# Performance work log

Measured on AMD Instinct MI355X. Metric: run time of the kernel, lower is better.

The kernel has to match this reference:

```python
import jax, jax.numpy as jnp
import numpy as np

B, S, D, H, F, L = 4, 2048, 768, 12, 3072, 4
DH = D // H  # dim_head = 64
EPS = 1e-5


def _layernorm(x, g, b):
    mu = jnp.mean(x, axis=-1, keepdims=True)
    var = jnp.var(x, axis=-1, keepdims=True)
    return (x - mu) * jax.lax.rsqrt(var + EPS) * g + b


def setup_inputs() -> dict:
    key = jax.random.key(0)
    ks = jax.random.split(key, 12)
    sc = 0.02
    x = jax.random.normal(ks[0], (B, S, D), dtype=jnp.float32)
    # causal mask: True where attention is disallowed (j > i)
    causal = jnp.triu(jnp.ones((S, S), dtype=bool), k=1)
    attn_mask = jnp.broadcast_to(causal, (B, S, S))
    Wq = jax.random.normal(ks[1], (L, D, D), dtype=jnp.float32) * sc
    Wk = jax.random.normal(ks[2], (L, D, D), dtype=jnp.float32) * sc
    Wv = jax.random.normal(ks[3], (L, D, D), dtype=jnp.float32) * sc
    Wo = jax.random.normal(ks[4], (L, D, D), dtype=jnp.float32) * sc
    bo = jnp.zeros((L, D), dtype=jnp.float32)
    ln1_g = jnp.ones((L, D), dtype=jnp.float32)
    ln1_b = jnp.zeros((L, D), dtype=jnp.float32)
    W1 = jax.random.normal(ks[5], (L, D, F), dtype=jnp.float32) * sc
    b1 = jnp.zeros((L, F), dtype=jnp.float32)
    W2 = jax.random.normal(ks[6], (L, F, D), dtype=jnp.float32) * sc
    b2 = jnp.zeros((L, D), dtype=jnp.float32)
    ln2_g = jnp.ones((L, D), dtype=jnp.float32)
    ln2_b = jnp.zeros((L, D), dtype=jnp.float32)
    return dict(x=x, attn_mask=attn_mask, Wq=Wq, Wk=Wk, Wv=Wv, Wo=Wo, bo=bo,
                ln1_g=ln1_g, ln1_b=ln1_b, W1=W1, b1=b1, W2=W2, b2=b2,
                ln2_g=ln2_g, ln2_b=ln2_b)


def _decoder_layer(x, mask, Wq, Wk, Wv, Wo, bo, ln1_g, ln1_b, W1, b1, W2, b2, ln2_g, ln2_b):
    # multi-head attention (dropout = identity in eval)
    q = (x @ Wq).reshape(B, S, H, DH).transpose(0, 2, 1, 3)  # (B,H,S,DH)
    k = (x @ Wk).reshape(B, S, H, DH).transpose(0, 2, 1, 3)
    v = (x @ Wv).reshape(B, S, H, DH).transpose(0, 2, 1, 3)
    a = jnp.einsum('bhqd,bhkd->bhqk', q, k) / jnp.sqrt(jnp.float32(DH))
    a = jnp.where(mask[:, None, :, :], jnp.float32(-1e9), a)
    p = jax.nn.softmax(a, axis=-1)
    av = jnp.einsum('bhqk,bhkd->bhqd', p, v)
    av = av.transpose(0, 2, 1, 3).reshape(B, S, D)
    attn_out = av @ Wo + bo
    h = _layernorm(x + attn_out, ln1_g, ln1_b)
    # FFN: Conv1d(kernel=1) == pointwise linear; exact GELU (torch F.gelu default)
    f = jax.nn.gelu(h @ W1 + b1, approximate=False) @ W2 + b2
    return _layernorm(h + f, ln2_g, ln2_b)


def reference(x, attn_mask, Wq, Wk, Wv, Wo, bo, ln1_g, ln1_b, W1, b1, W2, b2, ln2_g, ln2_b):
    for l in range(L):
        x = _decoder_layer(x, attn_mask, Wq[l], Wk[l], Wv[l], Wo[l], bo[l],
                           ln1_g[l], ln1_b[l], W1[l], b1[l], W2[l], b2[l],
                           ln2_g[l], ln2_b[l])
    return x
```

## Files before the change

kernel.cpp:

```cpp
#include <hip/hip_runtime.h>
#include <hip/hip_bf16.h>
#include <math.h>

#define BB 4
#define SS 2048
#define DD 768
#define HH 12
#define DHD 64
#define FF 3072
#define LL 4

typedef float f4 __attribute__((ext_vector_type(4)));
typedef float ffrag __attribute__((ext_vector_type(4)));
typedef __bf16 bf16x8 __attribute__((ext_vector_type(8)));
typedef __bf16 bf16x4 __attribute__((ext_vector_type(4)));

__device__ __forceinline__ void gld_lds16(const __bf16* g, __bf16* l) {
  __builtin_amdgcn_global_load_lds(
      (const __attribute__((address_space(1))) void*)g,
      (__attribute__((address_space(3))) void*)l, 16, 0, 0);
}

__device__ __forceinline__ float gelu_f(float x) {
  const float x2 = x * x;
  const float e = __expf(x * fmaf(-0.0713548162f, x2, -1.5957691216f));
  return x / (1.f + e);
}

template <int ACT, int WRITE_BF16, int MODE>
__global__ __launch_bounds__(256) void gemm_mfma(
    const __bf16* __restrict__ A,
    const __bf16* __restrict__ Bt,
    const float* __restrict__ bias,
    float* __restrict__ Cf,
    __bf16* __restrict__ Cb,
    __bf16* __restrict__ Vt,
    int M, int N, int K) {
  __shared__ __bf16 As[128 * 64];
  __shared__ __bf16 Bs[128 * 64];
  const int tid = threadIdx.x;
  const int lane = tid & 63;
  const int wid = tid >> 6;
  const int m0 = blockIdx.y * 128;
  const int n0 = blockIdx.x * 128;
  const int wm = (wid >> 1) * 64;
  const int wn = (wid & 1) * 64;

  ffrag acc[4][4];
#pragma unroll
  for (int i = 0; i < 4; ++i)
#pragma unroll
    for (int j = 0; j < 4; ++j) acc[i][j] = (ffrag)0.f;

  const int kr = lane >> 4;
  const int ml = lane & 15;
  const int quad = lane >> 4;

  for (int k0 = 0; k0 < K; k0 += 64) {
    __syncthreads();
#pragma unroll
    for (int it = 0; it < 4; ++it) {
      const int gidx = it * 256 + wid * 64 + lane;
      const int row = gidx >> 3;
      const int gl = (gidx & 7) ^ (row & 7);
      gld_lds16(A + (size_t)(m0 + row) * K + k0 + gl * 8,
                As + (size_t)(it * 256 + wid * 64) * 8);
      gld_lds16(Bt + (size_t)(n0 + row) * K + k0 + gl * 8,
                Bs + (size_t)(it * 256 + wid * 64) * 8);
    }
    __syncthreads();

#pragma unroll
    for (int kh = 0; kh < 64; kh += 32) {
      const int gb = (kh >> 3) + kr;
      bf16x8 af[4], bfr[4];
#pragma unroll
      for (int i = 0; i < 4; ++i) {
        const int ra = wm + i * 16 + ml;
        af[i] = *(const bf16x8*)(As + ra * 64 + ((gb ^ (ra & 7)) * 8));
        const int rb = wn + i * 16 + ml;
        bfr[i] = *(const bf16x8*)(Bs + rb * 64 + ((gb ^ (rb & 7)) * 8));
      }
#pragma unroll
      for (int i = 0; i < 4; ++i)
#pragma unroll
        for (int j = 0; j < 4; ++j) {
          if (MODE == 2)
            acc[i][j] = __builtin_amdgcn_mfma_f32_16x16x32_bf16(
                af[i], bfr[j], acc[i][j], 0, 0, 0);
          else
            acc[i][j] = __builtin_amdgcn_mfma_f32_16x16x32_bf16(
                bfr[j], af[i], acc[i][j], 0, 0, 0);
        }
    }
  }

  if (MODE == 2) {
    const int rq = quad * 4;
#pragma unroll
    for (int j = 0; j < 4; ++j) {
      const int col = n0 + wn + j * 16 + ml;
      const int hh = col >> 6, d = col & 63;
#pragma unroll
      for (int i = 0; i < 4; ++i) {
        const int row = m0 + wm + i * 16 + rq;
        const int bi = row >> 11, s = row & 2047;
        bf16x4 pk;
#pragma unroll
        for (int r = 0; r < 4; ++r) pk[r] = (__bf16)acc[i][j][r];
        *(bf16x4*)(Vt + ((size_t)(bi * HH + hh) * DHD + d) * SS + s) = pk;
      }
    }
  } else {
#pragma unroll
    for (int j = 0; j < 4; ++j) {
      const int ncol = n0 + wn + j * 16 + quad * 4;
      float4 b4 = make_float4(0.f, 0.f, 0.f, 0.f);
      if (MODE == 0 && bias) b4 = *(const float4*)(bias + ncol);
#pragma unroll
      for (int i = 0; i < 4; ++i) {
        const int mrow = m0 + wm + i * 16 + ml;
        float v0 = acc[i][j][0] + b4.x;
        float v1 = acc[i][j][1] + b4.y;
        float v2 = acc[i][j][2] + b4.z;
        float v3 = acc[i][j][3] + b4.w;
        if (ACT) {
          v0 = gelu_f(v0); v1 = gelu_f(v1);
          v2 = gelu_f(v2); v3 = gelu_f(v3);
        }
        if (MODE == 1) {
          bf16x4 pk;
          pk[0] = (__bf16)v0; pk[1] = (__bf16)v1;
          pk[2] = (__bf16)v2; pk[3] = (__bf16)v3;
          *(bf16x4*)(Cb + (size_t)mrow * 1536 + ncol) = pk;
        } else if (WRITE_BF16) {
          bf16x4 pk;
          pk[0] = (__bf16)v0; pk[1] = (__bf16)v1;
          pk[2] = (__bf16)v2; pk[3] = (__bf16)v3;
          *(bf16x4*)(Cb + (size_t)mrow * N + ncol) = pk;
        } else {
          float4 o; o.x = v0; o.y = v1; o.z = v2; o.w = v3;
          *(float4*)(Cf + (size_t)mrow * N + ncol) = o;
        }
      }
    }
  }
}

__global__ __launch_bounds__(256) void wtrans_kernel(
    const float* __restrict__ src, __bf16* __restrict__ dst, int R, int C,
    size_t src_ls, size_t dst_ls) {
  __shared__ float t[32][33];
  src += (size_t)blockIdx.z * src_ls;
  dst += (size_t)blockIdx.z * dst_ls;
  const int tx = threadIdx.x & 31;
  const int ty = threadIdx.x >> 5;
  const int r0 = blockIdx.y * 32;
  const int c0 = blockIdx.x * 32;
#pragma unroll
  for (int i = 0; i < 4; ++i)
    t[ty + i * 8][tx] = src[(size_t)(r0 + ty + i * 8) * C + c0 + tx];
  __syncthreads();
#pragma unroll
  for (int i = 0; i < 4; ++i)
    dst[(size_t)(c0 + ty + i * 8) * R + r0 + tx] = (__bf16)t[tx][ty + i * 8];
}

__global__ __launch_bounds__(256) void cvt_kernel(
    const float* __restrict__ x, __bf16* __restrict__ y, int n4) {
  const int i = blockIdx.x * 256 + threadIdx.x;
  if (i < n4) {
    const float4 v = *(const float4*)(x + (size_t)i * 4);
    bf16x4 o;
    o[0] = (__bf16)v.x; o[1] = (__bf16)v.y;
    o[2] = (__bf16)v.z; o[3] = (__bf16)v.w;
    *(bf16x4*)(y + (size_t)i * 4) = o;
  }
}

__global__ __launch_bounds__(256, 3) void attn_mfma(
    const __bf16* __restrict__ QK, const __bf16* __restrict__ VT,
    __bf16* __restrict__ O) {
  __shared__ __bf16 qs[64 * 64];
  __shared__ __bf16 ks[2][64 * 64];
  __shared__ __bf16 vts[2][64 * 64];
  __shared__ __bf16 ps[64 * 72];

  const int h = blockIdx.y;
  const int b = blockIdx.z;
  const int tid = threadIdx.x;
  const int lane = tid & 63;
  const int wid = tid >> 6;
  const int ml = lane & 15;
  const int quad = lane >> 4;
  const int wq = wid * 16;
  const size_t rowbase = (size_t)b * SS;
  const int hc = h * 64;
  const size_t vbase = (size_t)(b * HH + h) * DHD;
  const int NT = SS / 64;

  const int gidx0 = wid * 64 + lane;
  const int row0 = gidx0 >> 3;
  const int gl0 = (gidx0 & 7) ^ (row0 & 7);
  const int gidx1 = 256 + wid * 64 + lane;
  const int row1 = gidx1 >> 3;
  const int gl1 = (gidx1 & 7) ^ (row1 & 7);

  for (int ph = 0; ph < 2; ++ph) {
    const int qt = ph ? (NT - 1 - (int)blockIdx.x) : (int)blockIdx.x;
    const int q0 = qt * 64;

    __syncthreads();

    gld_lds16(QK + (rowbase + q0 + row0) * 1536 + hc + gl0 * 8,
              qs + (size_t)(wid * 64) * 8);
    gld_lds16(QK + (rowbase + q0 + row1) * 1536 + hc + gl1 * 8,
              qs + (size_t)(256 + wid * 64) * 8);
    gld_lds16(QK + (rowbase + row0) * 1536 + 768 + hc + gl0 * 8,
              ks[0] + (size_t)(wid * 64) * 8);
    gld_lds16(QK + (rowbase + row1) * 1536 + 768 + hc + gl1 * 8,
              ks[0] + (size_t)(256 + wid * 64) * 8);
    gld_lds16(VT + (vbase + row0) * SS + gl0 * 8, vts[0] + (size_t)(wid * 64) * 8);
    gld_lds16(VT + (vbase + row1) * SS + gl1 * 8, vts[0] + (size_t)(256 + wid * 64) * 8);

    ffrag oacc[4];
#pragma unroll
    for (int d = 0; d < 4; ++d) oacc[d] = (ffrag)0.f;
    float l_acc = 0.f;

    for (int ch = 0; ch <= qt; ++ch) {
      const int j0 = ch * 64;
      const int cur = ch & 1;
      __syncthreads();

      if (ch < qt) {
        const int jn = j0 + 64;
        gld_lds16(QK + (rowbase + jn + row0) * 1536 + 768 + hc + gl0 * 8,
                  ks[cur ^ 1] + (size_t)(wid * 64) * 8);
        gld_lds16(QK + (rowbase + jn + row1) * 1536 + 768 + hc + gl1 * 8,
                  ks[cur ^ 1] + (size_t)(256 + wid * 64) * 8);
        gld_lds16(VT + (vbase + row0) * SS + jn + gl0 * 8,
                  vts[cur ^ 1] + (size_t)(wid * 64) * 8);
        gld_lds16(VT + (vbase + row1) * SS + jn + gl1 * 8,
                  vts[cur ^ 1] + (size_t)(256 + wid * 64) * 8);
      }

      ffrag sa[4];
#pragma unroll
      for (int jt = 0; jt < 4; ++jt) sa[jt] = (ffrag)0.f;
#pragma unroll
      for (int kk = 0; kk < 2; ++kk) {
        const int gb = kk * 4 + quad;
        const int ra = wq + ml;
        const bf16x8 qf = *(const bf16x8*)(qs + ra * 64 + ((gb ^ (ra & 7)) * 8));
#pragma unroll
        for (int jt = 0; jt < 4; ++jt) {
          const int rb = jt * 16 + ml;
          const bf16x8 kf =
              *(const bf16x8*)(ks[cur] + rb * 64 + ((gb ^ (rb & 7)) * 8));
          sa[jt] = __builtin_amdgcn_mfma_f32_16x16x32_bf16(kf, qf, sa[jt], 0, 0, 0);
        }
      }

      const bool maskch = (j0 == q0);
      const int qrel = wq + ml;
      float lsum = 0.f;
      bf16x4 pk[4];
#pragma unroll
      for (int jt = 0; jt < 4; ++jt) {
#pragma unroll
        for (int r = 0; r < 4; ++r) {
          float p = __expf(sa[jt][r] * 0.125f);
          if (maskch && (jt * 16 + quad * 4 + r > qrel)) p = 0.f;
          lsum += p;
          pk[jt][r] = (__bf16)p;
        }
      }
      lsum += __shfl_xor(lsum, 16);
      lsum += __shfl_xor(lsum, 32);
      l_acc += lsum;

#pragma unroll
      for (int jt = 0; jt < 4; ++jt)
        *(bf16x4*)(ps + (size_t)(wq + ml) * 72 + jt * 16 + quad * 4) = pk[jt];

#pragma unroll
      for (int kk = 0; kk < 2; ++kk) {
        const bf16x8 ap =
            *(const bf16x8*)(ps + (size_t)(wq + ml) * 72 + kk * 32 + quad * 8);
        const int gb = kk * 4 + quad;
#pragma unroll
        for (int d = 0; d < 4; ++d) {
          const int rv = d * 16 + ml;
          const bf16x8 bv =
              *(const bf16x8*)(vts[cur] + rv * 64 + ((gb ^ (rv & 7)) * 8));
          oacc[d] = __builtin_amdgcn_mfma_f32_16x16x32_bf16(ap, bv, oacc[d], 0, 0, 0);
        }
      }
    }

#pragma unroll
    for (int r = 0; r < 4; ++r) {
      const int qloc = quad * 4 + r;
      const float lr = __shfl(l_acc, qloc);
      const float inv = 1.f / lr;
      const size_t row = rowbase + q0 + wq + qloc;
#pragma unroll
      for (int d = 0; d < 4; ++d)
        O[row * DD + hc + d * 16 + ml] = (__bf16)(oacc[d][r] * inv);
    }
  }
}

__global__ __launch_bounds__(256) void add_ln_kernel(
    const float* __restrict__ X, const float* __restrict__ R,
    const float* __restrict__ g, const float* __restrict__ be,
    float* __restrict__ O, __bf16* __restrict__ Ob) {
  const int row = blockIdx.x * 4 + (threadIdx.x >> 6);
  const int lane = threadIdx.x & 63;
  const float* xr = X + (size_t)row * DD;
  const float* rr = R + (size_t)row * DD;
  float v[12];
  float sum = 0.f;
#pragma unroll
  for (int i = 0; i < 3; ++i) {
    const float4 a = *(const float4*)(xr + i * 256 + lane * 4);
    const float4 c = *(const float4*)(rr + i * 256 + lane * 4);
    v[i * 4 + 0] = a.x + c.x;
    v[i * 4 + 1] = a.y + c.y;
    v[i * 4 + 2] = a.z + c.z;
    v[i * 4 + 3] = a.w + c.w;
    sum += v[i * 4 + 0] + v[i * 4 + 1] + v[i * 4 + 2] + v[i * 4 + 3];
  }
#pragma unroll
  for (int off = 32; off >= 1; off >>= 1) sum += __shfl_xor(sum, off);
  const float mean = sum * (1.f / 768.f);
  float sq = 0.f;
#pragma unroll
  for (int i = 0; i < 12; ++i) {
    const float d = v[i] - mean;
    sq += d * d;
  }
#pragma unroll
  for (int off = 32; off >= 1; off >>= 1) sq += __shfl_xor(sq, off);
  const float inv = rsqrtf(sq * (1.f / 768.f) + 1e-5f);
#pragma unroll
  for (int i = 0; i < 3; ++i) {
    const int c = i * 256 + lane * 4;
    const float4 gg = *(const float4*)(g + c);
    const float4 bb = *(const float4*)(be + c);
    float4 o;
    o.x = (v[i * 4 + 0] - mean) * inv * gg.x + bb.x;
    o.y = (v[i * 4 + 1] - mean) * inv * gg.y + bb.y;
    o.z = (v[i * 4 + 2] - mean) * inv * gg.z + bb.z;
    o.w = (v[i * 4 + 3] - mean) * inv * gg.w + bb.w;
    *(float4*)(O + (size_t)row * DD + c) = o;
    bf16x4 ob;
    ob[0] = (__bf16)o.x; ob[1] = (__bf16)o.y;
    ob[2] = (__bf16)o.z; ob[3] = (__bf16)o.w;
    *(bf16x4*)(Ob + (size_t)row * DD + c) = ob;
  }
}

extern "C" void kernel_launch(void* const* d_in, const int* in_sizes, int n_in,
                              void* d_out, int out_size, void* d_ws,
                              size_t ws_size, hipStream_t stream) {
  const float* x0   = (const float*)d_in[0];
  const float* Wq   = (const float*)d_in[2];
  const float* Wk   = (const float*)d_in[3];
  const float* Wv   = (const float*)d_in[4];
  const float* Wo   = (const float*)d_in[5];
  const float* bo   = (const float*)d_in[6];
  const float* ln1g = (const float*)d_in[7];
  const float* ln1b = (const float*)d_in[8];
  const float* W1   = (const float*)d_in[9];
  const float* b1   = (const float*)d_in[10];
  const float* W2   = (const float*)d_in[11];
  const float* b2   = (const float*)d_in[12];
  const float* ln2g = (const float*)d_in[13];
  const float* ln2b = (const float*)d_in[14];

  float* out = (float*)d_out;

  const size_t NTD = (size_t)BB * SS * DD;
  __bf16* qkbf = (__bf16*)d_ws;
  __bf16* vtbf = qkbf + (size_t)BB * SS * 1536;
  __bf16* xbf  = vtbf + NTD;
  __bf16* midbf = qkbf;
  float* aw   = (float*)(xbf + NTD);
  float* hbuf = aw + NTD;
  __bf16* btbf = (__bf16*)(hbuf + NTD);
  __bf16* hbf  = btbf + NTD;
  __bf16* wT   = hbf + NTD;

  const size_t WTL = 7077888;
  const size_t OQK = 0, OWO = (size_t)2304 * 768, OW1 = 2359296, OW2 = 4718592;

  const int M = BB * SS;
  const size_t DSQ = (size_t)DD * DD;

  cvt_kernel<<<(int)(NTD / 4 + 255) / 256, 256, 0, stream>>>(x0, xbf, (int)(NTD / 4));

  wtrans_kernel<<<dim3(24, 24, LL), 256, 0, stream>>>(Wq, wT + OQK, DD, DD, DSQ, WTL);
  wtrans_kernel<<<dim3(24, 24, LL), 256, 0, stream>>>(Wk, wT + (size_t)768 * 768, DD, DD, DSQ, WTL);
  wtrans_kernel<<<dim3(24, 24, LL), 256, 0, stream>>>(Wv, wT + (size_t)1536 * 768, DD, DD, DSQ, WTL);
  wtrans_kernel<<<dim3(24, 24, LL), 256, 0, stream>>>(Wo, wT + OWO, DD, DD, DSQ, WTL);
  wtrans_kernel<<<dim3(96, 24, LL), 256, 0, stream>>>(W1, wT + OW1, DD, FF, (size_t)DD * FF, WTL);
  wtrans_kernel<<<dim3(24, 96, LL), 256, 0, stream>>>(W2, wT + OW2, FF, DD, (size_t)FF * DD, WTL);

  for (int l = 0; l < LL; ++l) {
    const float* xin = (l == 0) ? x0 : out;
    const float* bol = bo + (size_t)l * DD;
    const float* g1 = ln1g + (size_t)l * DD;
    const float* be1 = ln1b + (size_t)l * DD;
    const float* b1l = b1 + (size_t)l * FF;
    const float* b2l = b2 + (size_t)l * DD;
    const float* g2 = ln2g + (size_t)l * DD;
    const float* be2 = ln2b + (size_t)l * DD;
    __bf16* wqkvT = wT + l * WTL + OQK;
    __bf16* woT   = wT + l * WTL + OWO;
    __bf16* w1T   = wT + l * WTL + OW1;
    __bf16* w2T   = wT + l * WTL + OW2;

    gemm_mfma<0, 1, 1><<<dim3(12, 64), 256, 0, stream>>>(
        xbf, wqkvT, nullptr, nullptr, qkbf, nullptr, M, 1536, DD);
    gemm_mfma<0, 0, 2><<<dim3(6, 64), 256, 0, stream>>>(
        xbf, wqkvT + (size_t)1536 * 768, nullptr, nullptr, nullptr, vtbf,
        M, 768, DD);
    attn_mfma<<<dim3(SS / 128, HH, BB), 256, 0, stream>>>(qkbf, vtbf, btbf);
    gemm_mfma<0, 0, 0><<<dim3(6, 64), 256, 0, stream>>>(
        btbf, woT, bol, aw, nullptr, nullptr, M, DD, DD);
    add_ln_kernel<<<M / 4, 256, 0, stream>>>(xin, aw, g1, be1, hbuf, hbf);
    gemm_mfma<1, 1, 0><<<dim3(24, 64), 256, 0, stream>>>(
        hbf, w1T, b1l, nullptr, midbf, nullptr, M, FF, DD);
    gemm_mfma<0, 0, 0><<<dim3(6, 64), 256, 0, stream>>>(
        midbf, w2T, b2l, aw, nullptr, nullptr, M, DD, FF);
    add_ln_kernel<<<M / 4, 256, 0, stream>>>(hbuf, aw, g2, be2, out, xbf);
  }
}
```

Before: 1.367 ms.

## Merge QKV GEMMs, split-K the W2 GEMM, and keep residual stream in bf16

Merges the QK and V projection GEMMs into one launch. Splits the K=3072 down-projection into two halves whose partial sums are added inside the second layernorm kernel. Drops the fp32 residual copies so the layernorms read the bf16 residual, and stores xbf in the output buffer. This aims to cut launches, raise block count for the narrow GEMM, and reduce fp32 memory traffic, at the cost of lower residual precision.

```diff
diff --git a/kernel.cpp b/kernel.cpp
--- a/kernel.cpp
+++ b/kernel.cpp
@@ -10,7 +10,6 @@
 #define FF 3072
 #define LL 4
 
-typedef float f4 __attribute__((ext_vector_type(4)));
 typedef float ffrag __attribute__((ext_vector_type(4)));
 typedef __bf16 bf16x8 __attribute__((ext_vector_type(8)));
 typedef __bf16 bf16x4 __attribute__((ext_vector_type(4)));
@@ -27,15 +26,59 @@
   return x / (1.f + e);
 }
 
-template <int ACT, int WRITE_BF16, int MODE>
-__global__ __launch_bounds__(256) void gemm_mfma(
-    const __bf16* __restrict__ A,
-    const __bf16* __restrict__ Bt,
-    const float* __restrict__ bias,
-    float* __restrict__ Cf,
-    __bf16* __restrict__ Cb,
-    __bf16* __restrict__ Vt,
-    int M, int N, int K) {
+template <int SWAP>
+__device__ __forceinline__ void gemm_core(
+    const __bf16* __restrict__ A, const __bf16* __restrict__ Bt,
+    __bf16* As, __bf16* Bs, int m0, int n0, int K, int kbeg, int kend,
+    int lane, int wid, ffrag (&acc)[4][4]) {
+  const int kr = lane >> 4;
+  const int ml = lane & 15;
+  const int wm = (wid >> 1) * 64;
+  const int wn = (wid & 1) * 64;
+  for (int k0 = kbeg; k0 < kend; k0 += 64) {
+    __syncthreads();
+#pragma unroll
+    for (int it = 0; it < 4; ++it) {
+      const int gidx = it * 256 + wid * 64 + lane;
+      const int row = gidx >> 3;
+      const int gl = (gidx & 7) ^ (row & 7);
+      gld_lds16(A + (size_t)(m0 + row) * K + k0 + gl * 8,
+                As + (size_t)(it * 256 + wid * 64) * 8);
+      gld_lds16(Bt + (size_t)(n0 + row) * K + k0 + gl * 8,
+                Bs + (size_t)(it * 256 + wid * 64) * 8);
+    }
+    __syncthreads();
+#pragma unroll
+    for (int kh = 0; kh < 2; ++kh) {
+      const int gb = kh * 4 + kr;
+      bf16x8 af[4], bfr[4];
+#pragma unroll
+      for (int i = 0; i < 4; ++i) {
+        const int ra = wm + i * 16 + ml;
+        af[i] = *(const bf16x8*)(As + ra * 64 + ((gb ^ (ra & 7)) * 8));
+        const int rb = wn + i * 16 + ml;
+        bfr[i] = *(const bf16x8*)(Bs + rb * 64 + ((gb ^ (rb & 7)) * 8));
+      }
+#pragma unroll
+      for (int i = 0; i < 4; ++i)
+#pragma unroll
+        for (int j = 0; j < 4; ++j) {
+          if (SWAP)
+            acc[i][j] = __builtin_amdgcn_mfma_f32_16x16x32_bf16(
+                bfr[j], af[i], acc[i][j], 0, 0, 0);
+          else
+            acc[i][j] = __builtin_amdgcn_mfma_f32_16x16x32_bf16(
+                af[i], bfr[j], acc[i][j], 0, 0, 0);
+        }
+    }
+  }
+}
+
+template <int ACT, int WRITE_BF16, int SPLITK>
+__global__ __launch_bounds__(256) void gemm_std(
+    const __bf16* __restrict__ A, const __bf16* __restrict__ Bt,
+    const float* __restrict__ bias, float* __restrict__ Cf,
+    __bf16* __restrict__ Cb, int M, int N, int K) {
   __shared__ __bf16 As[128 * 64];
   __shared__ __bf16 Bs[128 * 64];
   const int tid = threadIdx.x;
@@ -45,103 +88,105 @@
   const int n0 = blockIdx.x * 128;
   const int wm = (wid >> 1) * 64;
   const int wn = (wid & 1) * 64;
-
-  ffrag acc[4][4];
-#pragma unroll
-  for (int i = 0; i < 4; ++i)
-#pragma unroll
-    for (int j = 0; j < 4; ++j) acc[i][j] = (ffrag)0.f;
-
-  const int kr = lane >> 4;
   const int ml = lane & 15;
   const int quad = lane >> 4;
 
-  for (int k0 = 0; k0 < K; k0 += 64) {
-    __syncthreads();
-#pragma unroll
-    for (int it = 0; it < 4; ++it) {
-      const int gidx = it * 256 + wid * 64 + lane;
-      const int row = gidx >> 3;
-      const int gl = (gidx & 7) ^ (row & 7);
-      gld_lds16(A + (size_t)(m0 + row) * K + k0 + gl * 8,
-                As + (size_t)(it * 256 + wid * 64) * 8);
-      gld_lds16(Bt + (size_t)(n0 + row) * K + k0 + gl * 8,
-                Bs + (size_t)(it * 256 + wid * 64) * 8);
-    }
-    __syncthreads();
-
-#pragma unroll
-    for (int kh = 0; kh < 64; kh += 32) {
-      const int gb = (kh >> 3) + kr;
-      bf16x8 af[4], bfr[4];
+  int kbeg = 0, kend = K;
+  if (SPLITK) {
+    const int z = blockIdx.z;
+    const int half = K >> 1;
+    kbeg = z * half;
+    kend = kbeg + half;
+    Cf += (size_t)z * M * N;
+    if (z) bias = nullptr;
+  }
+
+  ffrag acc[4][4];
+#pragma unroll
+  for (int i = 0; i < 4; ++i)
+#pragma unroll
+    for (int j = 0; j < 4; ++j) acc[i][j] = (ffrag)0.f;
+
+  gemm_core<1>(A, Bt, As, Bs, m0, n0, K, kbeg, kend, lane, wid, acc);
+
+#pragma unroll
+  for (int j = 0; j < 4; ++j) {
+    const int ncol = n0 + wn + j * 16 + quad * 4;
+    float4 b4 = make_float4(0.f, 0.f, 0.f, 0.f);
+    if (bias) b4 = *(const float4*)(bias + ncol);
+#pragma unroll
+    for (int i = 0; i < 4; ++i) {
+      const int mrow = m0 + wm + i * 16 + ml;
+      float v0 = acc[i][j][0] + b4.x;
+      float v1 = acc[i][j][1] + b4.y;
+      float v2 = acc[i][j][2] + b4.z;
+      float v3 = acc[i][j][3] + b4.w;
+      if (ACT) {
+        v0 = gelu_f(v0); v1 = gelu_f(v1);
+        v2 = gelu_f(v2); v3 = gelu_f(v3);
+      }
+      if (WRITE_BF16) {
+        bf16x4 pk;
+        pk[0] = (__bf16)v0; pk[1] = (__bf16)v1;
+        pk[2] = (__bf16)v2; pk[3] = (__bf16)v3;
+        *(bf16x4*)(Cb + (size_t)mrow * N + ncol) = pk;
+      } else {
+        float4 o; o.x = v0; o.y = v1; o.z = v2; o.w = v3;
+        *(float4*)(Cf + (size_t)mrow * N + ncol) = o;
+      }
+    }
+  }
+}
+
+__global__ __launch_bounds__(256) void gemm_qkv(
+    const __bf16* __restrict__ A, const __bf16* __restrict__ Bt,
+    __bf16* __restrict__ QKb, __bf16* __restrict__ Vt, int M, int K) {
+  __shared__ __bf16 As[128 * 64];
+  __shared__ __bf16 Bs[128 * 64];
+  const int tid = threadIdx.x;
+  const int lane = tid & 63;
+  const int wid = tid >> 6;
+  const int m0 = blockIdx.y * 128;
+  const int n0 = blockIdx.x * 128;
+  const int wm = (wid >> 1) * 64;
+  const int wn = (wid & 1) * 64;
+  const int ml = lane & 15;
+  const int quad = lane >> 4;
+
+  ffrag acc[4][4];
+#pragma unroll
+  for (int i = 0; i < 4; ++i)
+#pragma unroll
+    for (int j = 0; j < 4; ++j) acc[i][j] = (ffrag)0.f;
+
+  if (n0 < 1536) {
+    gemm_core<1>(A, Bt, As, Bs, m0, n0, K, 0, K, lane, wid, acc);
+#pragma unroll
+    for (int j = 0; j < 4; ++j) {
+      const int ncol = n0 + wn + j * 16 + quad * 4;
 #pragma unroll
       for (int i = 0; i < 4; ++i) {
-        const int ra = wm + i * 16 + ml;
-        af[i] = *(const bf16x8*)(As + ra * 64 + ((gb ^ (ra & 7)) * 8));
-        const int rb = wn + i * 16 + ml;
-        bfr[i] = *(const bf16x8*)(Bs + rb * 64 + ((gb ^ (rb & 7)) * 8));
-      }
-#pragma unroll
-      for (int i = 0; i < 4; ++i)
-#pragma unroll
-        for (int j = 0; j < 4; ++j) {
-          if (MODE == 2)
-            acc[i][j] = __builtin_amdgcn_mfma_f32_16x16x32_bf16(
-                af[i], bfr[j], acc[i][j], 0, 0, 0);
-          else
-            acc[i][j] = __builtin_amdgcn_mfma_f32_16x16x32_bf16(
-                bfr[j], af[i], acc[i][j], 0, 0, 0);
-        }
-    }
-  }
-
-  if (MODE == 2) {
-    const int rq = quad * 4;
+        const int mrow = m0 + wm + i * 16 + ml;
+        bf16x4 pk;
+#pragma unroll
+        for (int r = 0; r < 4; ++r) pk[r] = (__bf16)acc[i][j][r];
+        *(bf16x4*)(QKb + (size_t)mrow * 1536 + ncol) = pk;
+      }
+    }
+  } else {
+    gemm_core<0>(A, Bt, As, Bs, m0, n0, K, 0, K, lane, wid, acc);
 #pragma unroll
     for (int j = 0; j < 4; ++j) {
-      const int col = n0 + wn + j * 16 + ml;
-      const int hh = col >> 6, d = col & 63;
+      const int vcol = n0 - 1536 + wn + j * 16 + ml;
+      const int hh = vcol >> 6, d = vcol & 63;
 #pragma unroll
       for (int i = 0; i < 4; ++i) {
-        const int row = m0 + wm + i * 16 + rq;
+        const int row = m0 + wm + i * 16 + quad * 4;
         const int bi = row >> 11, s = row & 2047;
         bf16x4 pk;
 #pragma unroll
         for (int r = 0; r < 4; ++r) pk[r] = (__bf16)acc[i][j][r];
         *(bf16x4*)(Vt + ((size_t)(bi * HH + hh) * DHD + d) * SS + s) = pk;
-      }
-    }
-  } else {
-#pragma unroll
-    for (int j = 0; j < 4; ++j) {
-      const int ncol = n0 + wn + j * 16 + quad * 4;
-      float4 b4 = make_float4(0.f, 0.f, 0.f, 0.f);
-      if (MODE == 0 && bias) b4 = *(const float4*)(bias + ncol);
-#pragma unroll
-      for (int i = 0; i < 4; ++i) {
-        const int mrow = m0 + wm + i * 16 + ml;
-        float v0 = acc[i][j][0] + b4.x;
-        float v1 = acc[i][j][1] + b4.y;
-        float v2 = acc[i][j][2] + b4.z;
-        float v3 = acc[i][j][3] + b4.w;
-        if (ACT) {
-          v0 = gelu_f(v0); v1 = gelu_f(v1);
-          v2 = gelu_f(v2); v3 = gelu_f(v3);
-        }
-        if (MODE == 1) {
-          bf16x4 pk;
-          pk[0] = (__bf16)v0; pk[1] = (__bf16)v1;
-          pk[2] = (__bf16)v2; pk[3] = (__bf16)v3;
-          *(bf16x4*)(Cb + (size_t)mrow * 1536 + ncol) = pk;
-        } else if (WRITE_BF16) {
-          bf16x4 pk;
-          pk[0] = (__bf16)v0; pk[1] = (__bf16)v1;
-          pk[2] = (__bf16)v2; pk[3] = (__bf16)v3;
-          *(bf16x4*)(Cb + (size_t)mrow * N + ncol) = pk;
-        } else {
-          float4 o; o.x = v0; o.y = v1; o.z = v2; o.w = v3;
-          *(float4*)(Cf + (size_t)mrow * N + ncol) = o;
-        }
       }
     }
   }
@@ -313,23 +358,28 @@
 }
 
 __global__ __launch_bounds__(256) void add_ln_kernel(
-    const float* __restrict__ X, const float* __restrict__ R,
-    const float* __restrict__ g, const float* __restrict__ be,
-    float* __restrict__ O, __bf16* __restrict__ Ob) {
+    const __bf16* __restrict__ X, const float* __restrict__ R1,
+    const float* __restrict__ R2, const float* __restrict__ g,
+    const float* __restrict__ be, float* __restrict__ Ofp,
+    __bf16* __restrict__ Ob) {
   const int row = blockIdx.x * 4 + (threadIdx.x >> 6);
   const int lane = threadIdx.x & 63;
-  const float* xr = X + (size_t)row * DD;
-  const float* rr = R + (size_t)row * DD;
+  const __bf16* xr = X + (size_t)row * DD;
+  const float* r1 = R1 + (size_t)row * DD;
+  const float* r2 = R2 ? R2 + (size_t)row * DD : nullptr;
   float v[12];
   float sum = 0.f;
 #pragma unroll
   for (int i = 0; i < 3; ++i) {
-    const float4 a = *(const float4*)(xr + i * 256 + lane * 4);
-    const float4 c = *(const float4*)(rr + i * 256 + lane * 4);
-    v[i * 4 + 0] = a.x + c.x;
-    v[i * 4 + 1] = a.y + c.y;
-    v[i * 4 + 2] = a.z + c.z;
-    v[i * 4 + 3] = a.w + c.w;
+    const int c = i * 256 + lane * 4;
+    const bf16x4 a = *(const bf16x4*)(xr + c);
+    const float4 b = *(const float4*)(r1 + c);
+    float4 c2 = make_float4(0.f, 0.f, 0.f, 0.f);
+    if (r2) c2 = *(const float4*)(r2 + c);
+    v[i * 4 + 0] = (float)a[0] + b.x + c2.x;
+    v[i * 4 + 1] = (float)a[1] + b.y + c2.y;
+    v[i * 4 + 2] = (float)a[2] + b.z + c2.z;
+    v[i * 4 + 3] = (float)a[3] + b.w + c2.w;
     sum += v[i * 4 + 0] + v[i * 4 + 1] + v[i * 4 + 2] + v[i * 4 + 3];
   }
 #pragma unroll
@@ -354,11 +404,13 @@
     o.y = (v[i * 4 + 1] - mean) * inv * gg.y + bb.y;
     o.z = (v[i * 4 + 2] - mean) * inv * gg.z + bb.z;
     o.w = (v[i * 4 + 3] - mean) * inv * gg.w + bb.w;
-    *(float4*)(O + (size_t)row * DD + c) = o;
-    bf16x4 ob;
-    ob[0] = (__bf16)o.x; ob[1] = (__bf16)o.y;
-    ob[2] = (__bf16)o.z; ob[3] = (__bf16)o.w;
-    *(bf16x4*)(Ob + (size_t)row * DD + c) = ob;
+    if (Ofp) *(float4*)(Ofp + (size_t)row * DD + c) = o;
+    if (Ob) {
+      bf16x4 ob;
+      ob[0] = (__bf16)o.x; ob[1] = (__bf16)o.y;
+      ob[2] = (__bf16)o.z; ob[3] = (__bf16)o.w;
+      *(bf16x4*)(Ob + (size_t)row * DD + c) = ob;
+    }
   }
 }
 
@@ -385,13 +437,12 @@
   const size_t NTD = (size_t)BB * SS * DD;
   __bf16* qkbf = (__bf16*)d_ws;
   __bf16* vtbf = qkbf + (size_t)BB * SS * 1536;
-  __bf16* xbf  = vtbf + NTD;
+  __bf16* btbf = vtbf + NTD;
   __bf16* midbf = qkbf;
-  float* aw   = (float*)(xbf + NTD);
-  float* hbuf = aw + NTD;
-  __bf16* btbf = (__bf16*)(hbuf + NTD);
   __bf16* hbf  = btbf + NTD;
-  __bf16* wT   = hbf + NTD;
+  float* aw    = (float*)(hbf + NTD);
+  __bf16* wT   = (__bf16*)(aw + 2 * NTD);
+  __bf16* xbf  = (__bf16*)d_out;
 
   const size_t WTL = 7077888;
   const size_t OQK = 0, OWO = (size_t)2304 * 768, OW1 = 2359296, OW2 = 4718592;
@@ -409,7 +460,6 @@
   wtrans_kernel<<<dim3(24, 96, LL), 256, 0, stream>>>(W2, wT + OW2, FF, DD, (size_t)FF * DD, WTL);
 
   for (int l = 0; l < LL; ++l) {
-    const float* xin = (l == 0) ? x0 : out;
     const float* bol = bo + (size_t)l * DD;
     const float* g1 = ln1g + (size_t)l * DD;
     const float* be1 = ln1b + (size_t)l * DD;
@@ -421,20 +471,19 @@
     __bf16* woT   = wT + l * WTL + OWO;
     __bf16* w1T   = wT + l * WTL + OW1;
     __bf16* w2T   = wT + l * WTL + OW2;
-
-    gemm_mfma<0, 1, 1><<<dim3(12, 64), 256, 0, stream>>>(
-        xbf, wqkvT, nullptr, nullptr, qkbf, nullptr, M, 1536, DD);
-    gemm_mfma<0, 0, 2><<<dim3(6, 64), 256, 0, stream>>>(
-        xbf, wqkvT + (size_t)1536 * 768, nullptr, nullptr, nullptr, vtbf,
-        M, 768, DD);
+    const bool last = (l == LL - 1);
+
+    gemm_qkv<<<dim3(18, 64), 256, 0, stream>>>(xbf, wqkvT, qkbf, vtbf, M, DD);
     attn_mfma<<<dim3(SS / 128, HH, BB), 256, 0, stream>>>(qkbf, vtbf, btbf);
-    gemm_mfma<0, 0, 0><<<dim3(6, 64), 256, 0, stream>>>(
-        btbf, woT, bol, aw, nullptr, nullptr, M, DD, DD);
-    add_ln_kernel<<<M / 4, 256, 0, stream>>>(xin, aw, g1, be1, hbuf, hbf);
-    gemm_mfma<1, 1, 0><<<dim3(24, 64), 256, 0, stream>>>(
-        hbf, w1T, b1l, nullptr, midbf, nullptr, M, FF, DD);
-    gemm_mfma<0, 0, 0><<<dim3(6, 64), 256, 0, stream>>>(
-        midbf, w2T, b2l, aw, nullptr, nullptr, M, DD, FF);
-    add_ln_kernel<<<M / 4, 256, 0, stream>>>(hbuf, aw, g2, be2, out, xbf);
-  }
-}
+    gemm_std<0, 0, 0><<<dim3(6, 64), 256, 0, stream>>>(
+        btbf, woT, bol, aw, nullptr, M, DD, DD);
+    add_ln_kernel<<<M / 4, 256, 0, stream>>>(
+        xbf, aw, nullptr, g1, be1, nullptr, hbf);
+    gemm_std<1, 1, 0><<<dim3(24, 64), 256, 0, stream>>>(
+        hbf, w1T, b1l, nullptr, midbf, M, FF, DD);
+    gemm_std<0, 0, 1><<<dim3(6, 64, 2), 256, 0, stream>>>(
+        midbf, w2T, b2l, aw, nullptr, M, DD, FF);
+    add_ln_kernel<<<M / 4, 256, 0, stream>>>(
+        hbf, aw, aw + NTD, g2, be2, last ? out : nullptr, last ? nullptr : xbf);
+  }
+}
```

After: 1.283 ms. 1.07x faster.
